# Kernel optimization log

Hardware: AMD Instinct MI355X
Metric: run time of the kernel (lower is better)

Reference implementation:

```python
import jax, jax.numpy as jnp
import numpy as np

DIM = 256; HEADS = 4; HD = DIM // HEADS; SCALE = HD ** -0.5
CBS = 4; CSTRIDE = 2; SBS = 4; NSEL = 16; WS = 7
B = 4; H = 64; W = 64


def _unfold(x, bs, stride):
    # x: (B,H,W,C) -> (B, nh*nw, C*bs*bs), flat channel order matches torch F.unfold
    # (index = c*bs*bs + kh*bs + kw)
    b, h, w, c = x.shape
    nh = (h - bs) // stride + 1
    nw = (w - bs) // stride + 1
    cols = [x[:, kh:kh + nh * stride:stride, kw:kw + nw * stride:stride, :]
            for kh in range(bs) for kw in range(bs)]
    p = jnp.stack(cols, axis=-1)  # (B,nh,nw,C,bs*bs)
    return p.reshape(b, nh * nw, c * bs * bs)


def _rel_pos_index(ws):
    coords = np.stack(np.meshgrid(np.arange(ws), np.arange(ws), indexing='ij')).reshape(2, -1)
    rel = (coords[:, :, None] - coords[:, None, :]).transpose(1, 2, 0).copy()
    rel[:, :, 0] += ws - 1
    rel[:, :, 1] += ws - 1
    rel[:, :, 0] *= 2 * ws - 1
    return jnp.asarray(rel.sum(-1))  # (ws*ws, ws*ws) int


def _mlp(x, w1, b1, w2, b2):
    return jax.nn.gelu(x @ w1 + b1, approximate=False) @ w2 + b2


def _window_attn(x, qkv_w, qkv_b, proj_w, proj_b, bias_table):
    b, c, h, w = x.shape
    ws = WS
    ph = (ws - h % ws) % ws
    pw = (ws - w % ws) % ws
    xp = jnp.pad(x, ((0, 0), (0, 0), (0, ph), (0, pw)))
    hp, wp = h + ph, w + pw
    xw = xp.reshape(b, c, hp // ws, ws, wp // ws, ws).transpose(0, 2, 4, 3, 5, 1).reshape(-1, ws * ws, c)
    bw = xw.shape[0]
    qkv = (xw @ qkv_w + qkv_b).reshape(bw, ws * ws, 3, HEADS, HD).transpose(2, 0, 3, 1, 4)
    q, k, v = qkv[0], qkv[1], qkv[2]
    attn = jnp.einsum('bhnd,bhmd->bhnm', q, k) * SCALE
    rpi = _rel_pos_index(ws)
    bias = bias_table[rpi.reshape(-1)].reshape(ws * ws, ws * ws, HEADS).transpose(2, 0, 1)
    attn = jax.nn.softmax(attn + bias[None], axis=-1)
    o = jnp.einsum('bhnm,bhmd->bhnd', attn, v).transpose(0, 2, 1, 3).reshape(bw, ws * ws, c)
    o = o @ proj_w + proj_b
    o = o.reshape(b, hp // ws, wp // ws, ws, ws, c).transpose(0, 5, 1, 3, 2, 4).reshape(b, c, hp, wp)
    return o[:, :, :h, :w]


def _forward(x, qkv_cmp_w, qkv_cmp_b, qkv_slc_w, qkv_slc_b,
             cmpk_w1, cmpk_b1, cmpk_w2, cmpk_b2,
             cmpv_w1, cmpv_b1, cmpv_w2, cmpv_b2, pos_embed,
             win_qkv_w, win_qkv_b, win_proj_w, win_proj_b, win_bias_table,
             proj_cmp_w, proj_cmp_b, proj_slc_w, proj_slc_b,
             gate_w1, gate_b1, gate_w2, gate_b2):
    b, c, h, w = x.shape
    n = h * w
    xs = x.reshape(b, c, n).transpose(0, 2, 1)  # (B,N,C)

    # --- compressed branch ---
    qkv = (xs @ qkv_cmp_w + qkv_cmp_b).reshape(b, n, 3, HEADS, HD).transpose(2, 0, 3, 1, 4)
    q_c, k_c, v_c = qkv[0], qkv[1], qkv[2]  # (B,heads,N,hd)
    k_flat = k_c.transpose(0, 2, 1, 3).reshape(b, n, c)
    v_flat = v_c.transpose(0, 2, 1, 3).reshape(b, n, c)
    fk = _unfold(k_flat.reshape(b, h, w, c), CBS, CSTRIDE)  # (B,nb,C*16)
    fv = _unfold(v_flat.reshape(b, h, w, c), CBS, CSTRIDE)
    nb = fk.shape[1]
    # replicate torch's reshape of the channel-major unfold vector into (bs*bs, dim)
    kpos = (fk.reshape(b, nb, CBS * CBS, c) + pos_embed[None]).reshape(b, nb, CBS * CBS * c)
    k_cmp = _mlp(kpos, cmpk_w1, cmpk_b1, cmpk_w2, cmpk_b2)  # (B,nb,C)
    v_cmp = _mlp(fv, cmpv_w1, cmpv_b1, cmpv_w2, cmpv_b2)
    kch = k_cmp.reshape(b, nb, HEADS, HD).transpose(0, 2, 1, 3)
    vch = v_cmp.reshape(b, nb, HEADS, HD).transpose(0, 2, 1, 3)
    attn_cmp = jax.nn.softmax(jnp.einsum('bhnd,bhmd->bhnm', q_c, kch) * SCALE, axis=-1)
    out_cmp = jnp.einsum('bhnm,bhmd->bhnd', attn_cmp, vch).transpose(0, 2, 1, 3).reshape(b, n, c)
    out_cmp = out_cmp @ proj_cmp_w + proj_cmp_b

    # --- selected branch ---
    qkv2 = (xs @ qkv_slc_w + qkv_slc_b).reshape(b, n, 3, HEADS, HD).transpose(2, 0, 3, 1, 4)
    q_s, k_s, v_s = qkv2[0], qkv2[1], qkv2[2]
    ks_flat = k_s.transpose(0, 2, 1, 3).reshape(b, n, c)
    vs_flat = v_s.transpose(0, 2, 1, 3).reshape(b, n, c)
    imp = attn_cmp.sum(axis=1).mean(axis=1)  # (B, nb)
    ns = min(NSEL, nb)
    _, idx = jax.lax.top_k(imp, ns)
    fkb = _unfold(ks_flat.reshape(b, h, w, c), SBS, SBS)
    fvb = _unfold(vs_flat.reshape(b, h, w, c), SBS, SBS)
    nb2 = fkb.shape[1]
    kb = fkb.reshape(b, nb2, SBS * SBS, c)
    vb = fvb.reshape(b, nb2, SBS * SBS, c)
    idx = jnp.clip(idx, 0, nb2 - 1)
    k_slc = jnp.take_along_axis(kb, idx[:, :, None, None], axis=1).reshape(b, ns * SBS * SBS, c)
    v_slc = jnp.take_along_axis(vb, idx[:, :, None, None], axis=1).reshape(b, ns * SBS * SBS, c)
    ksh = k_slc.reshape(b, -1, HEADS, HD).transpose(0, 2, 1, 3)
    vsh = v_slc.reshape(b, -1, HEADS, HD).transpose(0, 2, 1, 3)
    attn_slc = jax.nn.softmax(jnp.einsum('bhnd,bhmd->bhnm', q_s, ksh) * SCALE, axis=-1)
    out_slc = jnp.einsum('bhnm,bhmd->bhnd', attn_slc, vsh).transpose(0, 2, 1, 3).reshape(b, n, c)
    out_slc = out_slc @ proj_slc_w + proj_slc_b

    # --- window branch ---
    out_win = _window_attn(x, win_qkv_w, win_qkv_b, win_proj_w, win_proj_b, win_bias_table)
    out_win = out_win.reshape(b, c, n).transpose(0, 2, 1)

    # --- gated combination ---
    g = jax.nn.sigmoid(jax.nn.gelu(xs @ gate_w1 + gate_b1, approximate=False) @ gate_w2 + gate_b2)
    out = g[..., 0:1] * out_cmp + g[..., 1:2] * out_slc + g[..., 2:3] * out_win
    return out.transpose(0, 2, 1).reshape(b, c, h, w)


def setup_inputs() -> dict:
    key = jax.random.key(0)
    ks = jax.random.split(key, 16)
    s = 0.02
    d = {
        'x': jax.random.normal(ks[0], (B, DIM, H, W), jnp.float32),
        'qkv_cmp_w': jax.random.normal(ks[1], (DIM, 3 * DIM)) * s,
        'qkv_cmp_b': jnp.zeros((3 * DIM,)),
        'qkv_slc_w': jax.random.normal(ks[2], (DIM, 3 * DIM)) * s,
        'qkv_slc_b': jnp.zeros((3 * DIM,)),
        'cmpk_w1': jax.random.normal(ks[3], (DIM * CBS * CBS, 2 * DIM)) * s,
        'cmpk_b1': jnp.zeros((2 * DIM,)),
        'cmpk_w2': jax.random.normal(ks[4], (2 * DIM, DIM)) * s,
        'cmpk_b2': jnp.zeros((DIM,)),
        'cmpv_w1': jax.random.normal(ks[5], (DIM * CBS * CBS, 2 * DIM)) * s,
        'cmpv_b1': jnp.zeros((2 * DIM,)),
        'cmpv_w2': jax.random.normal(ks[6], (2 * DIM, DIM)) * s,
        'cmpv_b2': jnp.zeros((DIM,)),
        'pos_embed': jax.random.normal(ks[7], (1, CBS * CBS, DIM)) * s,
        'win_qkv_w': jax.random.normal(ks[8], (DIM, 3 * DIM)) * s,
        'win_qkv_b': jnp.zeros((3 * DIM,)),
        'win_proj_w': jax.random.normal(ks[9], (DIM, DIM)) * s,
        'win_proj_b': jnp.zeros((DIM,)),
        'win_bias_table': jax.random.normal(ks[10], ((2 * WS - 1) ** 2, HEADS)) * s,
        'proj_cmp_w': jax.random.normal(ks[11], (DIM, DIM)) * s,
        'proj_cmp_b': jnp.zeros((DIM,)),
        'proj_slc_w': jax.random.normal(ks[12], (DIM, DIM)) * s,
        'proj_slc_b': jnp.zeros((DIM,)),
        'gate_w1': jax.random.normal(ks[13], (DIM, DIM // 4)) * s,
        'gate_b1': jnp.zeros((DIM // 4,)),
        'gate_w2': jax.random.normal(ks[14], (DIM // 4, 3)) * s,
        'gate_b2': jnp.zeros((3,)),
    }
    return d


def reference(x, qkv_cmp_w, qkv_cmp_b, qkv_slc_w, qkv_slc_b,
              cmpk_w1, cmpk_b1, cmpk_w2, cmpk_b2,
              cmpv_w1, cmpv_b1, cmpv_w2, cmpv_b2, pos_embed,
              win_qkv_w, win_qkv_b, win_proj_w, win_proj_b, win_bias_table,
              proj_cmp_w, proj_cmp_b, proj_slc_w, proj_slc_b,
              gate_w1, gate_b1, gate_w2, gate_b2):
    return _forward(x, qkv_cmp_w, qkv_cmp_b, qkv_slc_w, qkv_slc_b,
                    cmpk_w1, cmpk_b1, cmpk_w2, cmpk_b2,
                    cmpv_w1, cmpv_b1, cmpv_w2, cmpv_b2, pos_embed,
                    win_qkv_w, win_qkv_b, win_proj_w, win_proj_b, win_bias_table,
                    proj_cmp_w, proj_cmp_b, proj_slc_w, proj_slc_b,
                    gate_w1, gate_b1, gate_w2, gate_b2)
```

## Files before the change

kernel.cpp:

```cpp
#include <hip/hip_runtime.h>
#include <stdint.h>
#include <stddef.h>


#define DEV __device__ __forceinline__

typedef __attribute__((ext_vector_type(8))) short short8;
typedef __attribute__((ext_vector_type(4))) float f32x4;
typedef unsigned short u16;

DEV u16 f2bf(float f){
    unsigned u = __float_as_uint(f);
    u += 0x7FFFu + ((u>>16)&1u);
    return (u16)(u>>16);
}
DEV float bf2f(u16 u){ return __uint_as_float(((unsigned)u)<<16); }

__global__ void k_xs(const float* __restrict__ x, u16* __restrict__ xh,
                     u16* __restrict__ xl){
    __shared__ float t[32][33];
    int b = blockIdx.z; int c0 = blockIdx.y*32; int n0 = blockIdx.x*32;
    int tx = threadIdx.x, ty = threadIdx.y;
    for(int i=ty;i<32;i+=8)
        t[i][tx] = x[((size_t)(b*256 + c0+i))*4096 + n0 + tx];
    __syncthreads();
    for(int i=ty;i<32;i+=8){
        float v = t[tx][i];
        u16 h = f2bf(v);
        size_t o = ((size_t)(b*4096 + n0+i))*256 + c0 + tx;
        xh[o] = h;
        xl[o] = f2bf(v - bf2f(h));
    }
}

__global__ void k_wt(const float* __restrict__ W, u16* __restrict__ WT,
                     int K, int N){
    __shared__ float t[32][33];
    int k0 = blockIdx.x*32, n0 = blockIdx.y*32;
    int tx = threadIdx.x, ty = threadIdx.y;
    for(int i=ty;i<32;i+=8)
        if(k0+i<K && n0+tx<N) t[i][tx] = W[(size_t)(k0+i)*N + n0+tx];
    __syncthreads();
    for(int i=ty;i<32;i+=8)
        if(n0+i<N && k0+tx<K) WT[(size_t)(n0+i)*K + k0+tx] = f2bf(t[tx][i]);
}

__global__ void k_wt2(const float* __restrict__ W, u16* __restrict__ Hi,
                      u16* __restrict__ Lo, int K, int N){
    __shared__ float t[32][33];
    int k0 = blockIdx.x*32, n0 = blockIdx.y*32;
    int tx = threadIdx.x, ty = threadIdx.y;
    for(int i=ty;i<32;i+=8)
        if(k0+i<K && n0+tx<N) t[i][tx] = W[(size_t)(k0+i)*N + n0+tx];
    __syncthreads();
    for(int i=ty;i<32;i+=8)
        if(n0+i<N && k0+tx<K){
            float v = t[tx][i];
            u16 h = f2bf(v);
            Hi[(size_t)(n0+i)*K + k0+tx] = h;
            Lo[(size_t)(n0+i)*K + k0+tx] = f2bf(v - bf2f(h));
        }
}

__global__ void k_vt(const float* __restrict__ vc, u16* __restrict__ vt,
                     int NK, int ldk){
    __shared__ float t[32][33];
    int b = blockIdx.z; int k0 = blockIdx.x*32; int c0 = blockIdx.y*32;
    int tx = threadIdx.x, ty = threadIdx.y;
    for(int i=ty;i<32;i+=8){
        int k = k0+i;
        t[i][tx] = (k < NK) ? vc[((size_t)(b*NK + k))*256 + c0 + tx] : 0.f;
    }
    __syncthreads();
    for(int i=ty;i<32;i+=8){
        int k = k0+tx;
        if(k < ldk)
            vt[((size_t)(b*256 + c0+i))*ldk + k] = f2bf(t[tx][i]);
    }
}

__global__ __launch_bounds__(256) void k_gemm(
        const float* __restrict__ A, const float* __restrict__ W,
        const float* __restrict__ bias, float* __restrict__ C,
        int M, int K, int Nn, int act)
{
    __shared__ float As[16][68];
    __shared__ float Bs[16][64];
    const int m0 = blockIdx.y*64, n0 = blockIdx.x*64;
    const int t = threadIdx.x, tx = t&15, ty = t>>4;
    float acc[4][4] = {};
    const int am = t>>2;
    const int ak = (t&3)*4;
    const bool arow_ok = (m0+am) < M;

    for(int k0=0;k0<K;k0+=16){
        float4 av = make_float4(0.f,0.f,0.f,0.f);
        if(arow_ok) av = *reinterpret_cast<const float4*>(&A[(size_t)(m0+am)*K + k0 + ak]);
        As[ak+0][am]=av.x; As[ak+1][am]=av.y; As[ak+2][am]=av.z; As[ak+3][am]=av.w;
        {
            int n = t&63, kb = t>>6;
            #pragma unroll
            for(int r=0;r<4;r++){
                int kk = r*4 + kb; float v = 0.f;
                if(n0+n < Nn) v = W[(size_t)(k0+kk)*Nn + n0+n];
                Bs[kk][n] = v;
            }
        }
        __syncthreads();
        #pragma unroll
        for(int kk=0;kk<16;kk++){
            float a0=As[kk][ty*4+0], a1=As[kk][ty*4+1], a2=As[kk][ty*4+2], a3=As[kk][ty*4+3];
            float b0=Bs[kk][tx*4+0], b1=Bs[kk][tx*4+1], b2=Bs[kk][tx*4+2], b3=Bs[kk][tx*4+3];
            acc[0][0]=fmaf(a0,b0,acc[0][0]); acc[0][1]=fmaf(a0,b1,acc[0][1]);
            acc[0][2]=fmaf(a0,b2,acc[0][2]); acc[0][3]=fmaf(a0,b3,acc[0][3]);
            acc[1][0]=fmaf(a1,b0,acc[1][0]); acc[1][1]=fmaf(a1,b1,acc[1][1]);
            acc[1][2]=fmaf(a1,b2,acc[1][2]); acc[1][3]=fmaf(a1,b3,acc[1][3]);
            acc[2][0]=fmaf(a2,b0,acc[2][0]); acc[2][1]=fmaf(a2,b1,acc[2][1]);
            acc[2][2]=fmaf(a2,b2,acc[2][2]); acc[2][3]=fmaf(a2,b3,acc[2][3]);
            acc[3][0]=fmaf(a3,b0,acc[3][0]); acc[3][1]=fmaf(a3,b1,acc[3][1]);
            acc[3][2]=fmaf(a3,b2,acc[3][2]); acc[3][3]=fmaf(a3,b3,acc[3][3]);
        }
        __syncthreads();
    }
    #pragma unroll
    for(int i=0;i<4;i++){
        int m = m0 + ty*4 + i;
        if(m >= M) continue;
        #pragma unroll
        for(int j=0;j<4;j++){
            int n = n0 + tx*4 + j;
            if(n >= Nn) continue;
            float v = acc[i][j] + (bias ? bias[n] : 0.f);
            if(act==1)      v = 0.5f*v*(1.0f + erff(v*0.70710678118654752f));
            else if(act==2) v = 1.0f/(1.0f + expf(-v));
            C[(size_t)m*Nn + n] = v;
        }
    }
}

template<int WM, int WN, int AM, int BMD, int NSPLIT, int OBF>
__global__ __launch_bounds__(256) void k_mgs(
        const float* __restrict__ Af, const u16* __restrict__ Ah,
        const u16* __restrict__ Al,
        const float* __restrict__ Bf, const u16* __restrict__ Bh,
        const u16* __restrict__ Bl,
        const float* __restrict__ bias, float* __restrict__ C,
        u16* __restrict__ Cb, u16* __restrict__ Cb2,
        int M, int N, int K, int lda, int ldb, int ldc, int act, float scale,
        long zsA, long zsB, long zsC)
{
    constexpr int BM = 32*WM, BN = 32*WN;
    constexpr bool SP = (NSPLIT == 3);
    const long zo = (long)blockIdx.z;
    if(AM==0){ Af += zo*zsA; } else { Ah += zo*zsA; if(AM==2) Al += zo*zsA; }
    if(BMD==0){ Bf += zo*zsB; } else { Bh += zo*zsB; if(BMD==2) Bl += zo*zsB; }
    if(OBF) Cb += zo*zsC; else C += zo*zsC;

    __shared__ u16 Ahi[BM*64];
    __shared__ u16 Alo[SP ? BM*64 : 8];
    __shared__ u16 Bhi[BN*64];
    __shared__ u16 Blo[SP ? BN*64 : 8];

    const int m0 = blockIdx.y*BM, n0 = blockIdx.x*BN;
    const int tid = threadIdx.x, lane = tid&63, wv = tid>>6;
    const int wm = (wv>>1)*(16*WM), wn = (wv&1)*(16*WN);
    f32x4 acc[WM][WN] = {};

    constexpr int TPR_A = 256/BM;
    constexpr int CH_A  = 8/TPR_A;
    const int arow = tid / TPR_A;
    const int acol0 = (tid % TPR_A)*(128/TPR_A);
    constexpr int TPR_B = 256/BN;
    constexpr int CH_B  = 8/TPR_B;
    const int brow = tid / TPR_B;
    const int bcol0 = (tid % TPR_B)*(128/TPR_B);

    for(int kt=0; kt<K; kt+=64){
        {
            const bool ok = (m0+arow) < M;
            #pragma unroll
            for(int c=0;c<CH_A;c++){
                int colbyte = acol0 + c*16;
                int e = colbyte>>1;
                const bool lok = ok && (kt + e + 8 <= K);
                short8 h = {}, l = {};
                if(AM==0){
                    float4 v0 = make_float4(0,0,0,0), v1 = v0;
                    if(lok){
                        const float* src = &Af[(size_t)(m0+arow)*lda + kt + e];
                        v0 = *reinterpret_cast<const float4*>(src);
                        v1 = *reinterpret_cast<const float4*>(src+4);
                    }
                    float vv[8] = {v0.x,v0.y,v0.z,v0.w,v1.x,v1.y,v1.z,v1.w};
                    #pragma unroll
                    for(int j=0;j<8;j++){
                        u16 hb = f2bf(vv[j]);
                        h[j] = (short)hb;
                        if(SP) l[j] = (short)f2bf(vv[j] - bf2f(hb));
                    }
                } else {
                    if(lok){
                        h = *reinterpret_cast<const short8*>(Ah + (size_t)(m0+arow)*lda + kt + e);
                        if(SP && AM==2)
                            l = *reinterpret_cast<const short8*>(Al + (size_t)(m0+arow)*lda + kt + e);
                    }
                }
                int byteoff = arow*128 + (colbyte ^ ((arow&7)<<4));
                *reinterpret_cast<short8*>(reinterpret_cast<char*>(Ahi)+byteoff) = h;
                if(SP)
                    *reinterpret_cast<short8*>(reinterpret_cast<char*>(Alo)+byteoff) = l;
            }
        }
        {
            const bool ok = (n0+brow) < N;
            #pragma unroll
            for(int c=0;c<CH_B;c++){
                int colbyte = bcol0 + c*16;
                int e = colbyte>>1;
                const bool lok = ok && (kt + e + 8 <= K);
                short8 h = {}, l = {};
                if(BMD==0){
                    float4 v0 = make_float4(0,0,0,0), v1 = v0;
                    if(lok){
                        const float* src = &Bf[(size_t)(n0+brow)*ldb + kt + e];
                        v0 = *reinterpret_cast<const float4*>(src);
                        v1 = *reinterpret_cast<const float4*>(src+4);
                    }
                    float vv[8] = {v0.x,v0.y,v0.z,v0.w,v1.x,v1.y,v1.z,v1.w};
                    #pragma unroll
                    for(int j=0;j<8;j++){
                        u16 hb = f2bf(vv[j]);
                        h[j] = (short)hb;
                        if(SP) l[j] = (short)f2bf(vv[j] - bf2f(hb));
                    }
                } else {
                    if(lok){
                        h = *reinterpret_cast<const short8*>(Bh + (size_t)(n0+brow)*ldb + kt + e);
                        if(SP && BMD==2)
                            l = *reinterpret_cast<const short8*>(Bl + (size_t)(n0+brow)*ldb + kt + e);
                    }
                }
                int byteoff = brow*128 + (colbyte ^ ((brow&7)<<4));
                *reinterpret_cast<short8*>(reinterpret_cast<char*>(Bhi)+byteoff) = h;
                if(SP)
                    *reinterpret_cast<short8*>(reinterpret_cast<char*>(Blo)+byteoff) = l;
            }
        }
        __syncthreads();
        __builtin_amdgcn_s_setprio(1);
        #pragma unroll
        for(int kb=0;kb<2;kb++){
            short8 ah[WM], al[WM], bh[WN], bl[WN];
            #pragma unroll
            for(int i=0;i<WM;i++){
                int ar = wm + i*16 + (lane&15);
                int ab = ar*128 + (((kb*64) + ((lane>>4)*16)) ^ ((ar&7)<<4));
                ah[i] = *reinterpret_cast<const short8*>(reinterpret_cast<const char*>(Ahi)+ab);
                if(SP)
                    al[i] = *reinterpret_cast<const short8*>(reinterpret_cast<const char*>(Alo)+ab);
            }
            #pragma unroll
            for(int i=0;i<WN;i++){
                int br = wn + i*16 + (lane&15);
                int bb = br*128 + (((kb*64) + ((lane>>4)*16)) ^ ((br&7)<<4));
                bh[i] = *reinterpret_cast<const short8*>(reinterpret_cast<const char*>(Bhi)+bb);
                if(SP)
                    bl[i] = *reinterpret_cast<const short8*>(reinterpret_cast<const char*>(Blo)+bb);
            }
            #pragma unroll
            for(int mi=0;mi<WM;mi++)
                #pragma unroll
                for(int ni=0;ni<WN;ni++){
                    if(SP){
                        acc[mi][ni] = __builtin_amdgcn_mfma_f32_16x16x32_bf16(
                                          al[mi], bh[ni], acc[mi][ni], 0, 0, 0);
                        acc[mi][ni] = __builtin_amdgcn_mfma_f32_16x16x32_bf16(
                                          ah[mi], bl[ni], acc[mi][ni], 0, 0, 0);
                    }
                    acc[mi][ni] = __builtin_amdgcn_mfma_f32_16x16x32_bf16(
                                      ah[mi], bh[ni], acc[mi][ni], 0, 0, 0);
                }
        }
        __builtin_amdgcn_s_setprio(0);
        __syncthreads();
    }
    #pragma unroll
    for(int mi=0;mi<WM;mi++){
        #pragma unroll
        for(int ni=0;ni<WN;ni++){
            int col = n0 + wn + ni*16 + (lane&15);
            if(col >= N) continue;
            int rowb = m0 + wm + mi*16 + ((lane>>4)*4);
            float bv = bias ? bias[col] : 0.f;
            #pragma unroll
            for(int r=0;r<4;r++){
                int m = rowb + r;
                if(m >= M) continue;
                float v = acc[mi][ni][r]*scale + bv;
                if(act==1)      v = 0.5f*v*(1.0f + erff(v*0.70710678118654752f));
                else if(act==2) v = 1.0f/(1.0f + expf(-v));
                if(OBF==2){
                    u16 hb = f2bf(v);
                    Cb [(size_t)m*ldc + col] = hb;
                    Cb2[(size_t)m*ldc + col] = f2bf(v - bf2f(hb));
                } else if(OBF==1){
                    Cb[(size_t)m*ldc + col] = f2bf(v);
                } else {
                    C [(size_t)m*ldc + col] = v;
                }
            }
        }
    }
}

template<int SPLIT, int IMP, int NKR, int NT, int LDV>
__global__ __launch_bounds__(256) void k_fattn(
    const float* __restrict__ Qg, const u16* __restrict__ Khg,
    const u16* __restrict__ Klg, const u16* __restrict__ VTg,
    float* __restrict__ Og, float* __restrict__ impp)
{
    const int qb = blockIdx.x, h = blockIdx.y, b = blockIdx.z;
    const int tid = threadIdx.x, lane = tid&63, wv = tid>>6;
    const int wm = wv*16;
    const int rgrp = lane>>4;
    const int cidx = lane&15;

    __shared__ u16 Qh[64*64];
    __shared__ u16 Ql[SPLIT?64*64:8];
    __shared__ u16 Kh[64*64];
    __shared__ u16 Kl[SPLIT?64*64:8];
    __shared__ u16 Pl[64*64];
    __shared__ u16 Vl[64*64];
    __shared__ float part[4][64];
    __shared__ float colacc[IMP? NT*64 : 8];

    {
        int row = tid>>2;
        int col0 = (tid&3)*32;
        const float* src = &Qg[((size_t)b*4096 + qb*64 + row)*768 + h*64];
        #pragma unroll
        for(int c=0;c<2;c++){
            int colbyte = col0 + c*16;
            int e = colbyte>>1;
            float4 v0 = *reinterpret_cast<const float4*>(src+e);
            float4 v1 = *reinterpret_cast<const float4*>(src+e+4);
            float vv[8]={v0.x,v0.y,v0.z,v0.w,v1.x,v1.y,v1.z,v1.w};
            short8 hh, ll;
            #pragma unroll
            for(int j=0;j<8;j++){
                u16 hb=f2bf(vv[j]); hh[j]=(short)hb;
                if(SPLIT) ll[j]=(short)f2bf(vv[j]-bf2f(hb));
            }
            int byteoff = row*128 + (colbyte ^ ((row&7)<<4));
            *reinterpret_cast<short8*>(reinterpret_cast<char*>(Qh)+byteoff)=hh;
            if(SPLIT)
                *reinterpret_cast<short8*>(reinterpret_cast<char*>(Ql)+byteoff)=ll;
        }
        if(IMP) for(int k=tid;k<NT*64;k+=256) colacc[k]=0.f;
    }

    float lsum[4] = {0.f,0.f,0.f,0.f};

    for(int t=0;t<NT;t++){
        const int kt = t*64;
        __syncthreads();
        {
            int row = tid>>2;
            int col0 = (tid&3)*32;
            const bool ok = (kt+row) < NKR;
            const u16* srch = &Khg[((size_t)b*NKR + kt + row)*256 + h*64];
            const u16* srcl = SPLIT ? &Klg[((size_t)b*NKR + kt + row)*256 + h*64] : nullptr;
            #pragma unroll
            for(int c=0;c<2;c++){
                int colbyte = col0 + c*16;
                int e = colbyte>>1;
                short8 hh={}, ll={};
                if(ok){
                    hh = *reinterpret_cast<const short8*>(srch+e);
                    if(SPLIT) ll = *reinterpret_cast<const short8*>(srcl+e);
                }
                int byteoff = row*128 + (colbyte ^ ((row&7)<<4));
                *reinterpret_cast<short8*>(reinterpret_cast<char*>(Kh)+byteoff)=hh;
                if(SPLIT)
                    *reinterpret_cast<short8*>(reinterpret_cast<char*>(Kl)+byteoff)=ll;
            }
        }
        __syncthreads();
        f32x4 acc[4] = {};
        __builtin_amdgcn_s_setprio(1);
        #pragma unroll
        for(int kb=0;kb<2;kb++){
            int koff = kb*64 + rgrp*16;
            int ar = wm + cidx;
            int ab = ar*128 + (koff ^ ((ar&7)<<4));
            short8 ah = *reinterpret_cast<const short8*>(reinterpret_cast<const char*>(Qh)+ab);
            short8 al;
            if(SPLIT) al = *reinterpret_cast<const short8*>(reinterpret_cast<const char*>(Ql)+ab);
            #pragma unroll
            for(int ni=0;ni<4;ni++){
                int br = ni*16 + cidx;
                int bb = br*128 + (koff ^ ((br&7)<<4));
                short8 bh = *reinterpret_cast<const short8*>(reinterpret_cast<const char*>(Kh)+bb);
                if(SPLIT){
                    short8 bl = *reinterpret_cast<const short8*>(reinterpret_cast<const char*>(Kl)+bb);
                    acc[ni] = __builtin_amdgcn_mfma_f32_16x16x32_bf16(al, bh, acc[ni], 0,0,0);
                    acc[ni] = __builtin_amdgcn_mfma_f32_16x16x32_bf16(ah, bl, acc[ni], 0,0,0);
                }
                acc[ni] = __builtin_amdgcn_mfma_f32_16x16x32_bf16(ah, bh, acc[ni], 0,0,0);
            }
        }
        __builtin_amdgcn_s_setprio(0);
        #pragma unroll
        for(int ni=0;ni<4;ni++){
            int col = kt + ni*16 + cidx;
            if(col < NKR){
                #pragma unroll
                for(int r=0;r<4;r++)
                    lsum[r] += __expf(acc[ni][r]*0.125f);
            }
        }
    }
    float inv[4];
    #pragma unroll
    for(int r=0;r<4;r++){
        float l = lsum[r];
        l += __shfl_xor(l,1); l += __shfl_xor(l,2);
        l += __shfl_xor(l,4); l += __shfl_xor(l,8);
        inv[r] = 1.f/l;
    }

    f32x4 acc_o[4] = {};
    for(int t=0;t<NT;t++){
        const int kt = t*64;
        __syncthreads();
        {
            int row = tid>>2;
            int col0 = (tid&3)*32;
            const bool ok = (kt+row) < NKR;
            const u16* srch = &Khg[((size_t)b*NKR + kt + row)*256 + h*64];
            const u16* srcl = SPLIT ? &Klg[((size_t)b*NKR + kt + row)*256 + h*64] : nullptr;
            #pragma unroll
            for(int c=0;c<2;c++){
                int colbyte = col0 + c*16;
                int e = colbyte>>1;
                short8 hh={}, ll={};
                if(ok){
                    hh = *reinterpret_cast<const short8*>(srch+e);
                    if(SPLIT) ll = *reinterpret_cast<const short8*>(srcl+e);
                }
                int byteoff = row*128 + (colbyte ^ ((row&7)<<4));
                *reinterpret_cast<short8*>(reinterpret_cast<char*>(Kh)+byteoff)=hh;
                if(SPLIT)
                    *reinterpret_cast<short8*>(reinterpret_cast<char*>(Kl)+byteoff)=ll;
            }
        }
        {
            int row = tid>>2;
            int col0 = (tid&3)*32;
            const u16* src = &VTg[((size_t)b*256 + h*64 + row)*LDV + kt];
            #pragma unroll
            for(int c=0;c<2;c++){
                int colbyte = col0 + c*16;
                int e = colbyte>>1;
                short8 hh={};
                if(kt + e + 8 <= LDV)
                    hh = *reinterpret_cast<const short8*>(src + e);
                int byteoff = row*128 + (colbyte ^ ((row&7)<<4));
                *reinterpret_cast<short8*>(reinterpret_cast<char*>(Vl)+byteoff)=hh;
            }
        }
        __syncthreads();
        f32x4 acc[4] = {};
        __builtin_amdgcn_s_setprio(1);
        #pragma unroll
        for(int kb=0;kb<2;kb++){
            int koff = kb*64 + rgrp*16;
            int ar = wm + cidx;
            int ab = ar*128 + (koff ^ ((ar&7)<<4));
            short8 ah = *reinterpret_cast<const short8*>(reinterpret_cast<const char*>(Qh)+ab);
            short8 al;
            if(SPLIT) al = *reinterpret_cast<const short8*>(reinterpret_cast<const char*>(Ql)+ab);
            #pragma unroll
            for(int ni=0;ni<4;ni++){
                int br = ni*16 + cidx;
                int bb = br*128 + (koff ^ ((br&7)<<4));
                short8 bh = *reinterpret_cast<const short8*>(reinterpret_cast<const char*>(Kh)+bb);
                if(SPLIT){
                    short8 bl = *reinterpret_cast<const short8*>(reinterpret_cast<const char*>(Kl)+bb);
                    acc[ni] = __builtin_amdgcn_mfma_f32_16x16x32_bf16(al, bh, acc[ni], 0,0,0);
                    acc[ni] = __builtin_amdgcn_mfma_f32_16x16x32_bf16(ah, bl, acc[ni], 0,0,0);
                }
                acc[ni] = __builtin_amdgcn_mfma_f32_16x16x32_bf16(ah, bh, acc[ni], 0,0,0);
            }
        }
        __builtin_amdgcn_s_setprio(0);
        float cs[4] = {0.f,0.f,0.f,0.f};
        #pragma unroll
        for(int ni=0;ni<4;ni++){
            #pragma unroll
            for(int r=0;r<4;r++){
                int col = kt + ni*16 + cidx;
                float p = 0.f;
                if(col < NKR)
                    p = __expf(acc[ni][r]*0.125f) * inv[r];
                int prow = wm + rgrp*4 + r;
                int pcol = ni*16 + cidx;
                int byteoff = prow*128 + ((pcol*2) ^ ((prow&7)<<4));
                *reinterpret_cast<u16*>(reinterpret_cast<char*>(Pl)+byteoff) = f2bf(p);
                if(IMP) cs[ni] += p;
            }
        }
        if(IMP){
            #pragma unroll
            for(int ni=0;ni<4;ni++){
                cs[ni] += __shfl_xor(cs[ni],16);
                cs[ni] += __shfl_xor(cs[ni],32);
            }
            if(rgrp==0){
                #pragma unroll
                for(int ni=0;ni<4;ni++)
                    part[wv][ni*16+cidx] = cs[ni];
            }
        }
        __syncthreads();
        if(IMP && tid < 64)
            colacc[kt+tid] += ((part[0][tid]+part[1][tid])+part[2][tid])+part[3][tid];
        __builtin_amdgcn_s_setprio(1);
        #pragma unroll
        for(int kb=0;kb<2;kb++){
            int koff = kb*64 + rgrp*16;
            int ar = wm + cidx;
            int ab = ar*128 + (koff ^ ((ar&7)<<4));
            short8 pa = *reinterpret_cast<const short8*>(reinterpret_cast<const char*>(Pl)+ab);
            #pragma unroll
            for(int ni=0;ni<4;ni++){
                int br = ni*16 + cidx;
                int bb = br*128 + (koff ^ ((br&7)<<4));
                short8 vb = *reinterpret_cast<const short8*>(reinterpret_cast<const char*>(Vl)+bb);
                acc_o[ni] = __builtin_amdgcn_mfma_f32_16x16x32_bf16(pa, vb, acc_o[ni], 0,0,0);
            }
        }
        __builtin_amdgcn_s_setprio(0);
    }
    __syncthreads();
    #pragma unroll
    for(int ni=0;ni<4;ni++){
        #pragma unroll
        for(int r=0;r<4;r++){
            int q = qb*64 + wm + rgrp*4 + r;
            int d = ni*16 + cidx;
            Og[((size_t)b*4096 + q)*256 + h*64 + d] = acc_o[ni][r];
        }
    }
    if(IMP){
        size_t base = ((size_t)((b*4+h)*64) + qb)*976;
        for(int k=tid; k<NT*64 && k<976; k+=256)
            impp[base+k] = colacc[k];
    }
}

__global__ void k_unfold2(const float* __restrict__ qkv, const float* __restrict__ pos,
                          u16* __restrict__ kh, u16* __restrict__ kl,
                          u16* __restrict__ vv){
    int row = blockIdx.x;
    int b = row / 961, blk = row % 961;
    int bi = blk / 31, bj = blk % 31;
    for(int j = threadIdx.x; j < 4096; j += 256){
        int ch = j >> 4;
        int khh = (j >> 2) & 3, kw = j & 3;
        int n = (bi*2 + khh)*64 + (bj*2 + kw);
        size_t base = ((size_t)(b*4096) + n)*768 + ch;
        float kv = qkv[base + 256] + pos[j];
        float va = qkv[base + 512];
        u16 h = f2bf(kv);
        kh[(size_t)row*4096 + j] = h;
        kl[(size_t)row*4096 + j] = f2bf(kv - bf2f(h));
        vv[(size_t)row*4096 + j] = f2bf(va);
    }
}

__global__ void k_imp_reduce(const float* __restrict__ impp, float* __restrict__ imp){
    __shared__ float part[4][64];
    int b = blockIdx.y;
    int k = blockIdx.x*64 + (threadIdx.x & 63);
    int rr = threadIdx.x >> 6;
    float s = 0.f;
    if(k < 976){
        for(int r=rr; r<256; r+=4)
            s += impp[((size_t)(b*256) + r)*976 + k];
    }
    part[rr][threadIdx.x & 63] = s;
    __syncthreads();
    if(threadIdx.x < 64 && k < 961){
        float t = ((part[0][threadIdx.x] + part[1][threadIdx.x])
                 + part[2][threadIdx.x]) + part[3][threadIdx.x];
        imp[b*961 + k] = t;
    }
}

__global__ __launch_bounds__(256) void k_topk(const float* __restrict__ imp,
                                              int* __restrict__ idx){
    int b = blockIdx.x;
    __shared__ float v[961];
    __shared__ float wvv[4];
    __shared__ int   wvi[4];
    int t = threadIdx.x;
    int lane = t & 63, wid = t >> 6;
    for(int i=t;i<961;i+=256) v[i] = imp[b*961+i];
    __syncthreads();
    for(int it=0; it<16; it++){
        float bv = -1e30f; int bi = 1<<30;
        for(int i=t;i<961;i+=256){
            float val = v[i];
            if(val > bv){ bv=val; bi=i; }
        }
        #pragma unroll
        for(int off=32; off>0; off>>=1){
            float ov = __shfl_xor(bv, off);
            int   oi = __shfl_xor(bi, off);
            if(ov > bv || (ov == bv && oi < bi)){ bv = ov; bi = oi; }
        }
        if(lane==0){ wvv[wid]=bv; wvi[wid]=bi; }
        __syncthreads();
        if(t==0){
            float gb=wvv[0]; int gi=wvi[0];
            #pragma unroll
            for(int w=1;w<4;w++){
                if(wvv[w]>gb || (wvv[w]==gb && wvi[w]<gi)){ gb=wvv[w]; gi=wvi[w]; }
            }
            idx[b*16+it] = gi;
            v[gi] = -1e30f;
        }
        __syncthreads();
    }
}

__global__ void k_gather_sel(const float* __restrict__ qkv2, const int* __restrict__ idx,
                             u16* __restrict__ Ks, float* __restrict__ Vs){
    int row = blockIdx.x;
    int b = row >> 8, tt = row & 255;
    int sel = tt >> 4, p = tt & 15;
    int blk = idx[b*16+sel]; if(blk > 255) blk = 255;
    int bi = blk >> 4, bj = blk & 15;
    int cc = threadIdx.x;
    int y = bi*4 + ((cc>>2)&3), xx = bj*4 + (cc&3);
    int ch = p*16 + (cc>>4);
    size_t src = ((size_t)(b*4096) + y*64 + xx)*768;
    Ks[(size_t)row*256 + cc] = f2bf(qkv2[src + 256 + ch]);
    Vs[(size_t)row*256 + cc] = qkv2[src + 512 + ch];
}

__global__ void k_xw(const u16* __restrict__ xh, u16* __restrict__ xw){
    int row = blockIdx.x;
    int wb = row / 49, t = row % 49;
    int b = wb / 100, wrem = wb % 100;
    int wy = wrem / 10, wx = wrem % 10;
    int ty = t / 7, tx = t % 7;
    int y = wy*7 + ty, xx = wx*7 + tx;
    int c = threadIdx.x;
    u16 v = 0;
    if(y < 64 && xx < 64) v = xh[((size_t)(b*4096) + y*64 + xx)*256 + c];
    xw[(size_t)row*256 + c] = v;
}

__global__ __launch_bounds__(64) void k_attn_win(
    const u16* __restrict__ qkvw, const float* __restrict__ btab,
    u16* __restrict__ outp)
{
    const int wb = blockIdx.x, h = blockIdx.y;
    const int lane = threadIdx.x;
    __shared__ float lk[49][64];
    __shared__ float lv[49][64];
    __shared__ float ls[49][51];
    __shared__ float lbias[169];
    for(int i=lane;i<169;i+=64) lbias[i] = btab[i*4 + h];
    for(int r=0;r<49;r++){
        lk[r][lane] = bf2f(qkvw[((size_t)(wb*49 + r))*768 + 256 + h*64 + lane]);
        lv[r][lane] = bf2f(qkvw[((size_t)(wb*49 + r))*768 + 512 + h*64 + lane]);
    }
    __syncthreads();
    if(lane < 49){
        const u16* qptr = &qkvw[((size_t)(wb*49 + lane))*768 + h*64];
        float qreg[64];
        #pragma unroll
        for(int d=0;d<64;++d) qreg[d] = bf2f(qptr[d]);
        int ih = lane/7, iw = lane%7;
        float m = -1e30f;
        for(int j=0;j<49;j++){
            float s0=0,s1=0,s2=0,s3=0;
            #pragma unroll
            for(int d=0; d<64; d+=4){
                s0 = fmaf(qreg[d+0], lk[j][d+0], s0);
                s1 = fmaf(qreg[d+1], lk[j][d+1], s1);
                s2 = fmaf(qreg[d+2], lk[j][d+2], s2);
                s3 = fmaf(qreg[d+3], lk[j][d+3], s3);
            }
            int jh=j/7, jw=j%7;
            float s = ((s0+s1)+(s2+s3))*0.125f + lbias[(ih-jh+6)*13 + (iw-jw+6)];
            ls[lane][j] = s;
            m = fmaxf(m, s);
        }
        float l = 0.f;
        for(int j=0;j<49;j++){ float p = __expf(ls[lane][j] - m); ls[lane][j] = p; l += p; }
        float inv = 1.f/l;
        u16* op = &outp[((size_t)(wb*49 + lane))*256 + h*64];
        for(int d=0;d<64;d++){
            float a0=0,a1=0;
            for(int j=0;j<48;j+=2){
                a0 = fmaf(ls[lane][j],   lv[j][d],   a0);
                a1 = fmaf(ls[lane][j+1], lv[j+1][d], a1);
            }
            a0 = fmaf(ls[lane][48], lv[48][d], a0);
            op[d] = f2bf((a0+a1)*inv);
        }
    }
}

__global__ void k_combine(const float* __restrict__ ocp, const float* __restrict__ osp,
                          const float* __restrict__ owp, const float* __restrict__ g,
                          float* __restrict__ out){
    __shared__ float tile[32][33];
    int b = blockIdx.z; int c0 = blockIdx.y*32, n0 = blockIdx.x*32;
    int tx = threadIdx.x, ty = threadIdx.y;
    for(int i=ty;i<32;i+=8){
        int n = n0 + i;
        float g0 = g[(size_t)(b*4096+n)*3 + 0];
        float g1 = g[(size_t)(b*4096+n)*3 + 1];
        float g2 = g[(size_t)(b*4096+n)*3 + 2];
        int y = n >> 6, xx = n & 63;
        int wy = y/7, ty2 = y%7, wx = xx/7, tx2 = xx%7;
        size_t wrow = (size_t)(b*100 + wy*10 + wx)*49 + ty2*7 + tx2;
        size_t base = ((size_t)(b*4096) + n)*256 + c0;
        float vc = ocp[base + tx];
        float vs = osp[base + tx];
        float vw = owp[wrow*256 + c0 + tx];
        tile[i][tx] = g0*vc + g1*vs + g2*vw;
    }
    __syncthreads();
    for(int i=ty;i<32;i+=8)
        out[((size_t)(b*256 + c0+i))*4096 + n0 + tx] = tile[tx][i];
}

extern "C" void kernel_launch(void* const* d_in, const int* in_sizes, int n_in,
                              void* d_out, int out_size, void* d_ws, size_t ws_size,
                              hipStream_t stream)
{
    typedef const float* fp;
    fp x          = (fp)d_in[0];
    fp qkv_cmp_w  = (fp)d_in[1];  fp qkv_cmp_b = (fp)d_in[2];
    fp qkv_slc_w  = (fp)d_in[3];  fp qkv_slc_b = (fp)d_in[4];
    fp cmpk_w1    = (fp)d_in[5];  fp cmpk_b1   = (fp)d_in[6];
    fp cmpk_w2    = (fp)d_in[7];  fp cmpk_b2   = (fp)d_in[8];
    fp cmpv_w1    = (fp)d_in[9];  fp cmpv_b1   = (fp)d_in[10];
    fp cmpv_w2    = (fp)d_in[11]; fp cmpv_b2   = (fp)d_in[12];
    fp pos_embed  = (fp)d_in[13];
    fp win_qkv_w  = (fp)d_in[14]; fp win_qkv_b = (fp)d_in[15];
    fp win_proj_w = (fp)d_in[16]; fp win_proj_b= (fp)d_in[17];
    fp win_btab   = (fp)d_in[18];
    fp proj_cmp_w = (fp)d_in[19]; fp proj_cmp_b= (fp)d_in[20];
    fp proj_slc_w = (fp)d_in[21]; fp proj_slc_b= (fp)d_in[22];
    fp gate_w1    = (fp)d_in[23]; fp gate_b1   = (fp)d_in[24];
    fp gate_w2    = (fp)d_in[25]; fp gate_b2   = (fp)d_in[26];
    (void)in_sizes; (void)n_in; (void)out_size;

    char* ws = (char*)d_ws;
    size_t off = 0;
    auto alloc = [&](size_t bytes)->size_t{
        size_t r = off; off += (bytes + 255) & ~(size_t)255; return r;
    };
    const size_t XSH  = alloc((size_t)16384*256*2);
    const size_t XSL  = alloc((size_t)16384*256*2);
    const size_t QKV  = alloc((size_t)16384*768*4);
    const size_t BIGA = alloc((size_t)4*4096*976*4);
    const size_t HID  = alloc((size_t)3844*512*4);
    const size_t KCH  = alloc((size_t)3844*256*2);
    const size_t KCL  = alloc((size_t)3844*256*2);
    const size_t VC   = alloc((size_t)3844*256*4);
    const size_t S_IMPP = (size_t)4096*976*4;
    const size_t S_OC   = (size_t)16384*256*4;
    const size_t S_PB   = (size_t)4*4096*976*2;
    const size_t POOL = alloc(S_IMPP + S_OC + S_OC + S_PB);
    const size_t IMP  = alloc((size_t)4*961*4);
    const size_t IDX  = alloc((size_t)4*16*4);
    const size_t KS   = alloc((size_t)4*256*256*2);
    const size_t VS   = alloc((size_t)4*256*256*4);
    const size_t G2   = alloc((size_t)16384*3*4);
    const size_t VTC  = alloc((size_t)4*256*976*2);
    const size_t VTS  = alloc((size_t)4*256*256*2);
    const size_t TQS  = alloc((size_t)768*256*2);
    const size_t TWQ  = alloc((size_t)768*256*2);
    const size_t TV1  = alloc((size_t)512*4096*2);
    const size_t TV2  = alloc((size_t)256*512*2);
    const size_t TPC  = alloc((size_t)256*256*2);
    const size_t TPS  = alloc((size_t)256*256*2);
    const size_t TWP  = alloc((size_t)256*256*2);
    const size_t TG1  = alloc((size_t)64*256*2);
    const size_t TQCH = alloc((size_t)768*256*2);
    const size_t TQCL = alloc((size_t)768*256*2);
    const size_t TK1H = alloc((size_t)512*4096*2);
    const size_t TK1L = alloc((size_t)512*4096*2);
    const size_t TK2H = alloc((size_t)256*512*2);
    const size_t TK2L = alloc((size_t)256*512*2);
    if(off > ws_size) return;

    u16*   p_xsh = (u16*)(ws + XSH);
    u16*   p_xsl = (u16*)(ws + XSL);
    float* p_qkv = (float*)(ws + QKV);
    u16*   p_bigb= (u16*)  (ws + BIGA);
    u16*   p_uv  = (u16*)  (ws + BIGA);
    float* p_oslc= (float*)(ws + BIGA);
    float* p_owp = (float*)(ws + BIGA + 20971520);
    float* p_hid = (float*)(ws + HID);
    u16*   p_kch = (u16*)(ws + KCH);
    u16*   p_kcl = (u16*)(ws + KCL);
    float* p_vc  = (float*)(ws + VC);
    float* p_impp= (float*)(ws + POOL);
    float* p_oc  = (float*)(ws + POOL + S_IMPP);
    float* p_ocp = (float*)(ws + POOL + S_IMPP + S_OC);
    u16*   p_ukh = (u16*)  (ws + POOL);
    u16*   p_ukl = p_ukh + (size_t)3844*4096;
    u16*   p_xwb = (u16*)  (ws + POOL);
    u16*   p_owin= (u16*)  (ws + POOL + S_IMPP);
    float* p_imp = (float*)(ws + IMP);
    int*   p_idx = (int*)  (ws + IDX);
    u16*   p_ks  = (u16*)(ws + KS);
    float* p_vs  = (float*)(ws + VS);
    float* p_g   = (float*)(ws + G2);
    u16*   p_vtc = (u16*)(ws + VTC);
    u16*   p_vts = (u16*)(ws + VTS);
    u16* t_qs = (u16*)(ws + TQS);
    u16* t_wq = (u16*)(ws + TWQ);
    u16* t_v1 = (u16*)(ws + TV1);
    u16* t_v2 = (u16*)(ws + TV2);
    u16* t_pc = (u16*)(ws + TPC);
    u16* t_ps = (u16*)(ws + TPS);
    u16* t_wp = (u16*)(ws + TWP);
    u16* t_g1 = (u16*)(ws + TG1);
    u16* t_qch= (u16*)(ws + TQCH);
    u16* t_qcl= (u16*)(ws + TQCL);
    u16* t_k1h= (u16*)(ws + TK1H);
    u16* t_k1l= (u16*)(ws + TK1L);
    u16* t_k2h= (u16*)(ws + TK2H);
    u16* t_k2l= (u16*)(ws + TK2L);

    auto wt = [&](fp W, u16* WT, int K, int Nn){
        k_wt<<<dim3((K+31)/32, (Nn+31)/32), dim3(32,8), 0, stream>>>(W, WT, K, Nn);
    };
    auto wt2 = [&](fp W, u16* H, u16* L, int K, int Nn){
        k_wt2<<<dim3((K+31)/32, (Nn+31)/32), dim3(32,8), 0, stream>>>(W, H, L, K, Nn);
    };

    wt(qkv_slc_w, t_qs, 256, 768);
    wt(win_qkv_w, t_wq, 256, 768);
    wt(cmpv_w1,   t_v1, 4096, 512);
    wt(cmpv_w2,   t_v2, 512, 256);
    wt(proj_cmp_w,t_pc, 256, 256);
    wt(proj_slc_w,t_ps, 256, 256);
    wt(win_proj_w,t_wp, 256, 256);
    wt(gate_w1,   t_g1, 256, 64);
    wt2(qkv_cmp_w, t_qch, t_qcl, 256, 768);
    wt2(cmpk_w1,   t_k1h, t_k1l, 4096, 512);
    wt2(cmpk_w2,   t_k2h, t_k2l, 512, 256);

    k_xs<<<dim3(128,8,4), dim3(32,8), 0, stream>>>(x, p_xsh, p_xsl);
    k_mgs<4,4,2,2,3,0><<<dim3(6,128), 256, 0, stream>>>(
        nullptr, p_xsh, p_xsl, nullptr, t_qch, t_qcl, qkv_cmp_b, p_qkv, nullptr, nullptr,
        16384, 768, 256, 256, 256, 768, 0, 1.0f, 0, 0, 0);
    k_unfold2<<<3844, 256, 0, stream>>>(p_qkv, pos_embed, p_ukh, p_ukl, p_uv);
    k_mgs<2,2,2,2,3,0><<<dim3(8,61), 256, 0, stream>>>(
        nullptr, p_ukh, p_ukl, nullptr, t_k1h, t_k1l, cmpk_b1, p_hid, nullptr, nullptr,
        3844, 512, 4096, 4096, 4096, 512, 1, 1.0f, 0, 0, 0);
    k_mgs<2,2,0,2,3,2><<<dim3(4,61), 256, 0, stream>>>(
        p_hid, nullptr, nullptr, nullptr, t_k2h, t_k2l, cmpk_b2, nullptr, p_kch, p_kcl,
        3844, 256, 512, 512, 512, 256, 0, 1.0f, 0, 0, 0);
    k_mgs<2,2,1,1,1,0><<<dim3(8,61), 256, 0, stream>>>(
        nullptr, p_uv, nullptr, nullptr, t_v1, nullptr, cmpv_b1, p_hid, nullptr, nullptr,
        3844, 512, 4096, 4096, 4096, 512, 1, 1.0f, 0, 0, 0);
    k_mgs<2,2,0,1,1,0><<<dim3(4,61), 256, 0, stream>>>(
        p_hid, nullptr, nullptr, nullptr, t_v2, nullptr, cmpv_b2, p_vc, nullptr, nullptr,
        3844, 256, 512, 512, 512, 256, 0, 1.0f, 0, 0, 0);
    k_vt<<<dim3(31,8,4), dim3(32,8), 0, stream>>>(p_vc, p_vtc, 961, 976);
    k_fattn<1,1,961,16,976><<<dim3(64,4,4), 256, 0, stream>>>(
        p_qkv, p_kch, p_kcl, p_vtc, p_oc, p_impp);
    k_imp_reduce<<<dim3(16,4), 256, 0, stream>>>(p_impp, p_imp);
    k_topk<<<4, 256, 0, stream>>>(p_imp, p_idx);
    k_mgs<4,4,0,1,1,0><<<dim3(2,128), 256, 0, stream>>>(
        p_oc, nullptr, nullptr, nullptr, t_pc, nullptr, proj_cmp_b, p_ocp, nullptr, nullptr,
        16384, 256, 256, 256, 256, 256, 0, 1.0f, 0, 0, 0);
    k_mgs<4,4,1,1,1,0><<<dim3(6,128), 256, 0, stream>>>(
        nullptr, p_xsh, nullptr, nullptr, t_qs, nullptr, qkv_slc_b, p_qkv, nullptr, nullptr,
        16384, 768, 256, 256, 256, 768, 0, 1.0f, 0, 0, 0);
    k_xw<<<19600, 256, 0, stream>>>(p_xsh, p_xwb);
    k_mgs<4,4,1,1,1,1><<<dim3(6,154), 256, 0, stream>>>(
        nullptr, p_xwb, nullptr, nullptr, t_wq, nullptr, win_qkv_b, nullptr, p_bigb, nullptr,
        19600, 768, 256, 256, 256, 768, 0, 1.0f, 0, 0, 0);
    k_attn_win<<<dim3(400,4), 64, 0, stream>>>(p_bigb, win_btab, p_owin);
    k_mgs<4,4,1,1,1,0><<<dim3(2,154), 256, 0, stream>>>(
        nullptr, p_owin, nullptr, nullptr, t_wp, nullptr, win_proj_b, p_owp, nullptr, nullptr,
        19600, 256, 256, 256, 256, 256, 0, 1.0f, 0, 0, 0);
    k_gather_sel<<<1024, 256, 0, stream>>>(p_qkv, p_idx, p_ks, p_vs);
    k_vt<<<dim3(8,8,4), dim3(32,8), 0, stream>>>(p_vs, p_vts, 256, 256);
    k_fattn<0,0,256,4,256><<<dim3(64,4,4), 256, 0, stream>>>(
        p_qkv, p_ks, nullptr, p_vts, p_oc, nullptr);
    k_mgs<4,4,0,1,1,0><<<dim3(2,128), 256, 0, stream>>>(
        p_oc, nullptr, nullptr, nullptr, t_ps, nullptr, proj_slc_b, p_oslc, nullptr, nullptr,
        16384, 256, 256, 256, 256, 256, 0, 1.0f, 0, 0, 0);
    k_mgs<2,2,1,1,1,0><<<dim3(1,256), 256, 0, stream>>>(
        nullptr, p_xsh, nullptr, nullptr, t_g1, nullptr, gate_b1, p_hid, nullptr, nullptr,
        16384, 64, 256, 256, 256, 64, 1, 1.0f, 0, 0, 0);
    k_gemm<<<dim3(1,256), 256, 0, stream>>>(p_hid, gate_w2, gate_b2, p_g,
                                            16384, 64, 3, 2);
    k_combine<<<dim3(128,8,4), dim3(32,8), 0, stream>>>(p_ocp, p_oslc, p_owp, p_g,
                                                        (float*)d_out);
}
```

Before: 828.4 us.

## Prefetch next K/V tiles into registers and use raw LDS barriers in attention

The attention kernel's K and V tile loads are split into a global-to-register prefetch and a register-to-LDS store. The next tile is fetched into registers while the current tile is being computed on, so global latency overlaps the MFMA work. The __syncthreads calls are replaced by an explicit lgkmcnt(0) wait plus s_barrier, which waits only on LDS traffic and not on outstanding global loads. This costs extra registers per thread for the prefetched tiles and relies on the hand-placed waits being correct.

```diff
diff --git a/kernel.cpp b/kernel.cpp
--- a/kernel.cpp
+++ b/kernel.cpp
@@ -15,6 +15,8 @@
     return (u16)(u>>16);
 }
 DEV float bf2f(u16 u){ return __uint_as_float(((unsigned)u)<<16); }
+
+#define LGKM0() asm volatile("s_waitcnt lgkmcnt(0)" ::: "memory")
 
 __global__ void k_xs(const float* __restrict__ x, u16* __restrict__ xh,
                      u16* __restrict__ xl){
@@ -334,13 +336,62 @@
     __shared__ float part[4][64];
     __shared__ float colacc[IMP? NT*64 : 8];
 
+    const int srow = tid>>2;
+    const int scol0 = (tid&3)*32;
+
+    short8 kh_r[2], kl_r[2], v_r[2];
+
+    auto LK = [&](int t){
+        const bool ok = (t*64 + srow) < NKR;
+        const u16* srch = &Khg[((size_t)b*NKR + t*64 + srow)*256 + h*64];
+        const u16* srcl = SPLIT ? &Klg[((size_t)b*NKR + t*64 + srow)*256 + h*64] : nullptr;
+        #pragma unroll
+        for(int c=0;c<2;c++){
+            int e = (scol0 + c*16)>>1;
+            short8 hh = {}, ll = {};
+            if(ok){
+                hh = *reinterpret_cast<const short8*>(srch+e);
+                if(SPLIT) ll = *reinterpret_cast<const short8*>(srcl+e);
+            }
+            kh_r[c] = hh;
+            if(SPLIT) kl_r[c] = ll;
+        }
+    };
+    auto WK = [&](){
+        #pragma unroll
+        for(int c=0;c<2;c++){
+            int colbyte = scol0 + c*16;
+            int byteoff = srow*128 + (colbyte ^ ((srow&7)<<4));
+            *reinterpret_cast<short8*>(reinterpret_cast<char*>(Kh)+byteoff) = kh_r[c];
+            if(SPLIT)
+                *reinterpret_cast<short8*>(reinterpret_cast<char*>(Kl)+byteoff) = kl_r[c];
+        }
+    };
+    auto LV = [&](int t){
+        const u16* src = &VTg[((size_t)b*256 + h*64 + srow)*LDV + t*64];
+        #pragma unroll
+        for(int c=0;c<2;c++){
+            int e = (scol0 + c*16)>>1;
+            short8 hh = {};
+            if(t*64 + e + 8 <= LDV)
+                hh = *reinterpret_cast<const short8*>(src + e);
+            v_r[c] = hh;
+        }
+    };
+    auto WV = [&](){
+        #pragma unroll
+        for(int c=0;c<2;c++){
+            int colbyte = scol0 + c*16;
+            int byteoff = srow*128 + (colbyte ^ ((srow&7)<<4));
+            *reinterpret_cast<short8*>(reinterpret_cast<char*>(Vl)+byteoff) = v_r[c];
+        }
+    };
+
     {
-        int row = tid>>2;
-        int col0 = (tid&3)*32;
-        const float* src = &Qg[((size_t)b*4096 + qb*64 + row)*768 + h*64];
+        const float* src = &Qg[((size_t)b*4096 + qb*64 + srow)*768 + h*64];
         #pragma unroll
         for(int c=0;c<2;c++){
-            int colbyte = col0 + c*16;
+            int colbyte = scol0 + c*16;
             int e = colbyte>>1;
             float4 v0 = *reinterpret_cast<const float4*>(src+e);
             float4 v1 = *reinterpret_cast<const float4*>(src+e+4);
@@ -351,7 +402,7 @@
                 u16 hb=f2bf(vv[j]); hh[j]=(short)hb;
                 if(SPLIT) ll[j]=(short)f2bf(vv[j]-bf2f(hb));
             }
-            int byteoff = row*128 + (colbyte ^ ((row&7)<<4));
+            int byteoff = srow*128 + (colbyte ^ ((srow&7)<<4));
             *reinterpret_cast<short8*>(reinterpret_cast<char*>(Qh)+byteoff)=hh;
             if(SPLIT)
                 *reinterpret_cast<short8*>(reinterpret_cast<char*>(Ql)+byteoff)=ll;
@@ -361,31 +412,15 @@
 
     float lsum[4] = {0.f,0.f,0.f,0.f};
 
+    LK(0);
     for(int t=0;t<NT;t++){
         const int kt = t*64;
-        __syncthreads();
-        {
-            int row = tid>>2;
-            int col0 = (tid&3)*32;
-            const bool ok = (kt+row) < NKR;
-            const u16* srch = &Khg[((size_t)b*NKR + kt + row)*256 + h*64];
-            const u16* srcl = SPLIT ? &Klg[((size_t)b*NKR + kt + row)*256 + h*64] : nullptr;
-            #pragma unroll
-            for(int c=0;c<2;c++){
-                int colbyte = col0 + c*16;
-                int e = colbyte>>1;
-                short8 hh={}, ll={};
-                if(ok){
-                    hh = *reinterpret_cast<const short8*>(srch+e);
-                    if(SPLIT) ll = *reinterpret_cast<const short8*>(srcl+e);
-                }
-                int byteoff = row*128 + (colbyte ^ ((row&7)<<4));
-                *reinterpret_cast<short8*>(reinterpret_cast<char*>(Kh)+byteoff)=hh;
-                if(SPLIT)
-                    *reinterpret_cast<short8*>(reinterpret_cast<char*>(Kl)+byteoff)=ll;
-            }
-        }
-        __syncthreads();
+        LGKM0();
+        __builtin_amdgcn_s_barrier();
+        WK();
+        if(t+1<NT) LK(t+1);
+        LGKM0();
+        __builtin_amdgcn_s_barrier();
         f32x4 acc[4] = {};
         __builtin_amdgcn_s_setprio(1);
         #pragma unroll
@@ -430,46 +465,15 @@
     }
 
     f32x4 acc_o[4] = {};
+    LK(0); LV(0);
     for(int t=0;t<NT;t++){
         const int kt = t*64;
-        __syncthreads();
-        {
-            int row = tid>>2;
-            int col0 = (tid&3)*32;
-            const bool ok = (kt+row) < NKR;
-            const u16* srch = &Khg[((size_t)b*NKR + kt + row)*256 + h*64];
-            const u16* srcl = SPLIT ? &Klg[((size_t)b*NKR + kt + row)*256 + h*64] : nullptr;
-            #pragma unroll
-            for(int c=0;c<2;c++){
-                int colbyte = col0 + c*16;
-                int e = colbyte>>1;
-                short8 hh={}, ll={};
-                if(ok){
-                    hh = *reinterpret_cast<const short8*>(srch+e);
-                    if(SPLIT) ll = *reinterpret_cast<const short8*>(srcl+e);
-                }
-                int byteoff = row*128 + (colbyte ^ ((row&7)<<4));
-                *reinterpret_cast<short8*>(reinterpret_cast<char*>(Kh)+byteoff)=hh;
-                if(SPLIT)
-                    *reinterpret_cast<short8*>(reinterpret_cast<char*>(Kl)+byteoff)=ll;
-            }
-        }
-        {
-            int row = tid>>2;
-            int col0 = (tid&3)*32;
-            const u16* src = &VTg[((size_t)b*256 + h*64 + row)*LDV + kt];
-            #pragma unroll
-            for(int c=0;c<2;c++){
-                int colbyte = col0 + c*16;
-                int e = colbyte>>1;
-                short8 hh={};
-                if(kt + e + 8 <= LDV)
-                    hh = *reinterpret_cast<const short8*>(src + e);
-                int byteoff = row*128 + (colbyte ^ ((row&7)<<4));
-                *reinterpret_cast<short8*>(reinterpret_cast<char*>(Vl)+byteoff)=hh;
-            }
-        }
-        __syncthreads();
+        LGKM0();
+        __builtin_amdgcn_s_barrier();
+        WK(); WV();
+        if(t+1<NT){ LK(t+1); LV(t+1); }
+        LGKM0();
+        __builtin_amdgcn_s_barrier();
         f32x4 acc[4] = {};
         __builtin_amdgcn_s_setprio(1);
         #pragma unroll
@@ -522,7 +526,8 @@
                     part[wv][ni*16+cidx] = cs[ni];
             }
         }
-        __syncthreads();
+        LGKM0();
+        __builtin_amdgcn_s_barrier();
         if(IMP && tid < 64)
             colacc[kt+tid] += ((part[0][tid]+part[1][tid])+part[2][tid])+part[3][tid];
         __builtin_amdgcn_s_setprio(1);
```

After: 816.8 us. No clear change (-1.4%).
